# Kernel optimization log

Hardware: AMD Instinct MI355X
Metric: run time of the kernel (lower is better)

Reference implementation:

```python
import jax, jax.numpy as jnp
import numpy as np

VOCAB, EMBED, HIDDEN, NCLS = 50257, 1024, 4096, 3
B, S = 4096, 128


def ternary_quant(w):
    # Per-tensor ternary quantization: scale = mean |w|, weights in {-s, 0, +s}.
    s = jnp.mean(jnp.abs(w))
    return jnp.round(jnp.clip(w / s, -1.0, 1.0)) * s


def layer_norm(x, g, b, eps=1e-5):
    mu = jnp.mean(x, axis=-1, keepdims=True)
    var = jnp.mean(jnp.square(x - mu), axis=-1, keepdims=True)
    return (x - mu) * jax.lax.rsqrt(var + eps) * g + b


def setup_inputs() -> dict:
    key = jax.random.key(0)
    ks = jax.random.split(key, 12)
    input_ids = jax.random.randint(ks[0], (B, S), 0, VOCAB, dtype=jnp.int32)
    emb = jax.random.normal(ks[1], (VOCAB, EMBED), dtype=jnp.float32) * 0.02
    emb = emb.at[0].set(0.0)  # padding_idx=0
    w1 = jax.random.normal(ks[2], (HIDDEN, EMBED), dtype=jnp.float32) * 0.02
    b1 = jnp.zeros((HIDDEN,), jnp.float32)
    w2 = jax.random.normal(ks[3], (HIDDEN // 2, HIDDEN), dtype=jnp.float32) * 0.02
    b2 = jnp.zeros((HIDDEN // 2,), jnp.float32)
    w3 = jax.random.normal(ks[4], (NCLS, HIDDEN // 2), dtype=jnp.float32) * 0.02
    b3 = jnp.zeros((NCLS,), jnp.float32)
    g1 = jnp.ones((HIDDEN,), jnp.float32)
    beta1 = jnp.zeros((HIDDEN,), jnp.float32)
    g2 = jnp.ones((HIDDEN // 2,), jnp.float32)
    beta2 = jnp.zeros((HIDDEN // 2,), jnp.float32)
    return dict(input_ids=input_ids, emb=emb, w1=w1, b1=b1, w2=w2, b2=b2,
                w3=w3, b3=b3, g1=g1, beta1=beta1, g2=g2, beta2=beta2)


def reference(input_ids, emb, w1, b1, w2, b2, w3, b3, g1, beta1, g2, beta2):
    x = emb[input_ids]                                   # (B, S, E)
    mask = (input_ids != 0).astype(x.dtype)[..., None]   # (B, S, 1)
    x = jnp.sum(x * mask, axis=1) / jnp.clip(jnp.sum(mask, axis=1), 1.0)  # (B, E)
    h = jax.nn.gelu(layer_norm(x @ ternary_quant(w1).T + b1, g1, beta1), approximate=False)
    h = jax.nn.gelu(layer_norm(h @ ternary_quant(w2).T + b2, g2, beta2), approximate=False)
    logits = h @ ternary_quant(w3).T + b3                # (B, 3)
    return logits
```

## Files before the change

kernel.cpp:

```cpp
#include <hip/hip_runtime.h>
#include <cstdint>
#include <cstddef>


#define GAS __attribute__((address_space(1)))
#define LAS __attribute__((address_space(3)))

typedef __bf16 bf16x8 __attribute__((ext_vector_type(8)));
typedef float  f32x4  __attribute__((ext_vector_type(4)));
typedef unsigned short u16x8 __attribute__((ext_vector_type(8)));

__device__ __forceinline__ unsigned short f2bf(float f) {
    unsigned int u = __float_as_uint(f);
    u += 0x7FFFu + ((u >> 16) & 1u);
    return (unsigned short)(u >> 16);
}
__device__ __forceinline__ float bf2f(unsigned short h) {
    return __uint_as_float(((unsigned int)h) << 16);
}

static constexpr int BB = 4096;
static constexpr int SS = 128;
static constexpr int EE = 1024;
static constexpr int HH = 4096;
static constexpr int H2D = 2048;
static constexpr int VOCAB = 50257;

static constexpr size_t OFF_S    = 0;
static constexpr size_t OFF_X    = 4096;
static constexpr size_t SZ_X     = (size_t)BB * EE * 2;
static constexpr size_t OFF_EMBH = OFF_X + SZ_X;
static constexpr size_t SZ_EMBH  = (size_t)VOCAB * EE * 2;
static constexpr size_t OFF_Q1   = OFF_EMBH;
static constexpr size_t OFF_Q2   = OFF_Q1 + (size_t)HH * EE * 2;
static constexpr size_t OFF_C    = OFF_Q2 + (size_t)H2D * HH * 2;
static constexpr size_t OFF_H1   = OFF_EMBH + SZ_EMBH;
static constexpr size_t OFF_H2   = OFF_Q1;


__global__ void zero_sums(double* s) {
    if (threadIdx.x < 3) s[threadIdx.x] = 0.0;
}

__global__ __launch_bounds__(256) void prep_kernel(const float* __restrict__ e,
                                                   unsigned short* __restrict__ o,
                                                   const float* __restrict__ w1,
                                                   const float* __restrict__ w2,
                                                   const float* __restrict__ w3,
                                                   double* __restrict__ sums) {
    const int bid = blockIdx.x;
    const int tid = threadIdx.x;
    if (bid < 4096) {
        const int n8 = (VOCAB * EE) / 8;
        for (int i = bid * 256 + tid; i < n8; i += 4096 * 256) {
            const float4 v0 = ((const float4*)e)[2 * i];
            const float4 v1 = ((const float4*)e)[2 * i + 1];
            union { unsigned short u[8]; uint4 q; } r;
            r.u[0] = f2bf(v0.x); r.u[1] = f2bf(v0.y); r.u[2] = f2bf(v0.z); r.u[3] = f2bf(v0.w);
            r.u[4] = f2bf(v1.x); r.u[5] = f2bf(v1.y); r.u[6] = f2bf(v1.z); r.u[7] = f2bf(v1.w);
            ((uint4*)o)[i] = r.q;
        }
        return;
    }
    const float* w; int n; double* out; int b0; int nb;
    if (bid < 5120)      { w = w1; n = HH * EE;  out = sums + 0; b0 = bid - 4096; nb = 1024; }
    else if (bid < 7168) { w = w2; n = H2D * HH; out = sums + 1; b0 = bid - 5120; nb = 2048; }
    else                 { w = w3; n = 3 * H2D;  out = sums + 2; b0 = bid - 7168; nb = 24;   }
    const int lane = tid & 63, wid = tid >> 6;
    double acc = 0.0;
    for (int i = b0 * 256 + tid; i < n; i += nb * 256)
        acc += (double)fabsf(w[i]);
    for (int off = 32; off; off >>= 1) acc += __shfl_down(acc, off);
    __shared__ double r[4];
    if (lane == 0) r[wid] = acc;
    __syncthreads();
    if (tid == 0) atomicAdd(out, r[0] + r[1] + r[2] + r[3]);
}

__global__ __launch_bounds__(256) void quant_all(const float* __restrict__ w1,
                                                 const float* __restrict__ w2,
                                                 const double* __restrict__ sums,
                                                 unsigned short* __restrict__ q1,
                                                 unsigned short* __restrict__ q2) {
    const int bid = blockIdx.x;
    const float* w; int n; unsigned short* q; int b0; int nb; double ssum; double dn;
    if (bid < 4096) { w = w1; n = HH * EE;  q = q1; b0 = bid;        nb = 4096; ssum = sums[0]; dn = (double)(HH) * EE; }
    else            { w = w2; n = H2D * HH; q = q2; b0 = bid - 4096; nb = 8192; ssum = sums[1]; dn = (double)(H2D) * HH; }
    const float inv_s = (float)(dn / ssum);
    for (int i = b0 * 256 + threadIdx.x; i < n; i += nb * 256) {
        float t = w[i] * inv_s;
        t = fminf(1.f, fmaxf(-1.f, t));
        q[i] = f2bf(rintf(t));
    }
}

__global__ __launch_bounds__(256) void pool_kernel(const int* __restrict__ ids,
                                                   const unsigned short* __restrict__ embh,
                                                   unsigned short* __restrict__ X) {
    const int tid = threadIdx.x;
    const int row = tid >> 7;
    const int t   = tid & 127;
    __shared__ int sid[256];
    __shared__ int sorted_ids[2][128];
    __shared__ int cnt[2][64];
    __shared__ int pos[2][64];
    __shared__ int nz[2];
    sid[tid] = ids[(size_t)blockIdx.x * 256 + tid];
    if (tid < 128) ((int*)cnt)[tid] = 0;
    if (tid < 2) nz[tid] = 0;
    __syncthreads();
    const int myid = sid[tid];
    const int ph = myid >> 10;
    atomicAdd(&cnt[row][ph], 1);
    if (myid != 0) atomicAdd(&nz[row], 1);
    __syncthreads();
    if (tid < 2) {
        int s = 0;
        #pragma unroll
        for (int p = 0; p < 64; ++p) { pos[tid][p] = s; s += cnt[tid][p]; }
    }
    __syncthreads();
    const int where = atomicAdd(&pos[row][ph], 1);
    sorted_ids[row][where] = myid;
    __syncthreads();

    const int col = t * 8;
    float a[8] = {};
    #pragma unroll 8
    for (int s = 0; s < 128; ++s) {
        const int id = sorted_ids[row][s];
        const u16x8 v = *(const u16x8*)(embh + (size_t)id * EE + col);
        #pragma unroll
        for (int j = 0; j < 8; ++j) a[j] += bf2f(v[j]);
    }
    const int c = nz[row];
    const float inv = 1.f / (float)(c ? c : 1);
    u16x8 ov;
    #pragma unroll
    for (int j = 0; j < 8; ++j) ov[j] = f2bf(a[j] * inv);
    const int b = blockIdx.x * 2 + row;
    *(u16x8*)(X + (size_t)b * EE + col) = ov;
}

__global__ __launch_bounds__(256) void gemm_bt(const unsigned short* __restrict__ A,
                                               const unsigned short* __restrict__ B,
                                               float* __restrict__ C, int M, int N, int K) {
    __shared__ unsigned short sA[128 * 32];
    __shared__ unsigned short sB[128 * 32];
    const int tid  = threadIdx.x;
    const int wid  = tid >> 6;
    const int lane = tid & 63;
    const int wm = wid >> 1, wn = wid & 1;
    const int quad = lane >> 4;
    const int l16  = lane & 15;
    const int mBase = blockIdx.y * 128;
    const int nBase = blockIdx.x * 128;

    f32x4 acc[4][4] = {};

    const int srow = tid >> 2;
    const int scol = (tid & 3) * 8;
    const size_t aOff0 = (size_t)(mBase + srow) * K + scol;
    const size_t aOff1 = aOff0 + (size_t)64 * K;
    const size_t bOff0 = (size_t)(nBase + srow) * K + scol;
    const size_t bOff1 = bOff0 + (size_t)64 * K;
    unsigned short* ldsA0 = &sA[wid * 512];
    unsigned short* ldsA1 = &sA[2048 + wid * 512];
    unsigned short* ldsB0 = &sB[wid * 512];
    unsigned short* ldsB1 = &sB[2048 + wid * 512];

    for (int k0 = 0; k0 < K; k0 += 32) {
        __syncthreads();
        __builtin_amdgcn_global_load_lds((const GAS void*)(A + aOff0 + k0), (LAS void*)ldsA0, 16, 0, 0);
        __builtin_amdgcn_global_load_lds((const GAS void*)(A + aOff1 + k0), (LAS void*)ldsA1, 16, 0, 0);
        __builtin_amdgcn_global_load_lds((const GAS void*)(B + bOff0 + k0), (LAS void*)ldsB0, 16, 0, 0);
        __builtin_amdgcn_global_load_lds((const GAS void*)(B + bOff1 + k0), (LAS void*)ldsB1, 16, 0, 0);
        __syncthreads();

        bf16x8 af[4], bfr[4];
        #pragma unroll
        for (int i = 0; i < 4; ++i) {
            const int rowA = wm * 64 + i * 16 + l16;
            af[i]  = *(const bf16x8*)(&sA[rowA * 32 + quad * 8]);
            const int rowB = wn * 64 + i * 16 + l16;
            bfr[i] = *(const bf16x8*)(&sB[rowB * 32 + quad * 8]);
        }
        #pragma unroll
        for (int i = 0; i < 4; ++i)
            #pragma unroll
            for (int j = 0; j < 4; ++j)
                acc[i][j] = __builtin_amdgcn_mfma_f32_16x16x32_bf16(af[i], bfr[j], acc[i][j], 0, 0, 0);
    }

    #pragma unroll
    for (int i = 0; i < 4; ++i) {
        const int row0 = mBase + wm * 64 + i * 16 + quad * 4;
        #pragma unroll
        for (int j = 0; j < 4; ++j) {
            const int col = nBase + wn * 64 + j * 16 + l16;
            #pragma unroll
            for (int r = 0; r < 4; ++r)
                C[(size_t)(row0 + r) * N + col] = acc[i][j][r];
        }
    }
}

__global__ __launch_bounds__(256) void ln_gelu_kernel(const float* __restrict__ Cm,
                                                      const double* __restrict__ ssum, double nw,
                                                      const float* __restrict__ bias,
                                                      const float* __restrict__ gamma,
                                                      const float* __restrict__ beta,
                                                      unsigned short* __restrict__ H, int N) {
    __shared__ float buf[4096];
    __shared__ float redS[4], redQ[4];
    const int row = blockIdx.x, tid = threadIdx.x;
    const int lane = tid & 63, wid = tid >> 6;
    const float s = (float)(ssum[0] / nw);
    float ps = 0.f, pq = 0.f;
    for (int c = tid; c < N; c += 256) {
        const float y = Cm[(size_t)row * N + c] * s + bias[c];
        buf[c] = y;
        ps += y; pq += y * y;
    }
    for (int o = 32; o; o >>= 1) { ps += __shfl_down(ps, o); pq += __shfl_down(pq, o); }
    if (lane == 0) { redS[wid] = ps; redQ[wid] = pq; }
    __syncthreads();
    const float sum = redS[0] + redS[1] + redS[2] + redS[3];
    const float sq  = redQ[0] + redQ[1] + redQ[2] + redQ[3];
    const float mu  = sum / (float)N;
    float var = sq / (float)N - mu * mu;
    var = fmaxf(var, 0.f);
    const float inv = rsqrtf(var + 1e-5f);
    for (int c = tid; c < N; c += 256) {
        const float y = (buf[c] - mu) * inv * gamma[c] + beta[c];
        const float g = 0.5f * y * (1.f + erff(y * 0.70710678118654752f));
        H[(size_t)row * N + c] = f2bf(g);
    }
}

__global__ __launch_bounds__(256) void final_kernel(const unsigned short* __restrict__ H2,
                                                    const float* __restrict__ w3,
                                                    const double* __restrict__ ssum,
                                                    const float* __restrict__ b3,
                                                    float* __restrict__ out) {
    const int row = blockIdx.x, tid = threadIdx.x;
    const int lane = tid & 63, wid = tid >> 6;
    const float inv_s3 = (float)((double)(3 * H2D) / ssum[0]);
    float a0 = 0.f, a1 = 0.f, a2 = 0.f;
    for (int k = tid; k < H2D; k += 256) {
        const float h = bf2f(H2[(size_t)row * H2D + k]);
        const float q0 = rintf(fminf(1.f, fmaxf(-1.f, w3[k] * inv_s3)));
        const float q1 = rintf(fminf(1.f, fmaxf(-1.f, w3[H2D + k] * inv_s3)));
        const float q2 = rintf(fminf(1.f, fmaxf(-1.f, w3[2 * H2D + k] * inv_s3)));
        a0 += h * q0; a1 += h * q1; a2 += h * q2;
    }
    for (int o = 32; o; o >>= 1) {
        a0 += __shfl_down(a0, o); a1 += __shfl_down(a1, o); a2 += __shfl_down(a2, o);
    }
    __shared__ float r[3][4];
    if (lane == 0) { r[0][wid] = a0; r[1][wid] = a1; r[2][wid] = a2; }
    __syncthreads();
    if (tid < 3) {
        const float s3 = (float)(ssum[0] / (double)(3 * H2D));
        out[(size_t)row * 3 + tid] =
            (r[tid][0] + r[tid][1] + r[tid][2] + r[tid][3]) * s3 + b3[tid];
    }
}


extern "C" void kernel_launch(void* const* d_in, const int* in_sizes, int n_in,
                              void* d_out, int out_size, void* d_ws, size_t ws_size,
                              hipStream_t stream) {
    const int*   ids = (const int*)d_in[0];
    const float* emb = (const float*)d_in[1];
    const float* w1  = (const float*)d_in[2];
    const float* b1  = (const float*)d_in[3];
    const float* w2  = (const float*)d_in[4];
    const float* b2  = (const float*)d_in[5];
    const float* w3  = (const float*)d_in[6];
    const float* b3  = (const float*)d_in[7];
    const float* g1  = (const float*)d_in[8];
    const float* be1 = (const float*)d_in[9];
    const float* g2  = (const float*)d_in[10];
    const float* be2 = (const float*)d_in[11];
    float* out = (float*)d_out;
    char* ws = (char*)d_ws;

    double*         sums = (double*)(ws + OFF_S);
    unsigned short* X    = (unsigned short*)(ws + OFF_X);
    unsigned short* embh = (unsigned short*)(ws + OFF_EMBH);
    unsigned short* q1   = (unsigned short*)(ws + OFF_Q1);
    unsigned short* q2   = (unsigned short*)(ws + OFF_Q2);
    float*          Cbuf = (float*)(ws + OFF_C);
    unsigned short* H1   = (unsigned short*)(ws + OFF_H1);
    unsigned short* H2   = (unsigned short*)(ws + OFF_H2);

    zero_sums<<<1, 64, 0, stream>>>(sums);
    prep_kernel<<<7192, 256, 0, stream>>>(emb, embh, w1, w2, w3, sums);
    pool_kernel<<<BB / 2, 256, 0, stream>>>(ids, embh, X);

    quant_all<<<12288, 256, 0, stream>>>(w1, w2, sums, q1, q2);

    gemm_bt<<<dim3(HH / 128, BB / 128), 256, 0, stream>>>(X, q1, Cbuf, BB, HH, EE);
    ln_gelu_kernel<<<BB, 256, 0, stream>>>(Cbuf, sums + 0, (double)HH * (double)EE,
                                           b1, g1, be1, H1, HH);
    gemm_bt<<<dim3(H2D / 128, BB / 128), 256, 0, stream>>>(H1, q2, Cbuf, BB, H2D, HH);
    ln_gelu_kernel<<<BB, 256, 0, stream>>>(Cbuf, sums + 1, (double)H2D * (double)HH,
                                           b2, g2, be2, H2, H2D);
    final_kernel<<<BB, 256, 0, stream>>>(H2, w3, sums + 2, b3, out);
}
```

Before: 723.0 us.

## Gather fp32 embeddings directly and drop full-vocab bf16 conversion pass

Removes the pass that converted the whole 50257x1024 embedding table to bf16 and instead has the pooling kernel read fp32 rows directly, sorting ids with finer buckets for locality. The weight abs-sum reduction becomes a two-stage deterministic partial-sum reduction with float4 loads instead of double atomics, and quantization processes eight elements per thread with vectorized loads and stores. This avoids reading and writing roughly 300MB for the table conversion, at the cost of doubling the bytes gathered per embedding row during pooling.

```diff
diff --git a/kernel.cpp b/kernel.cpp
--- a/kernel.cpp
+++ b/kernel.cpp
@@ -27,54 +27,54 @@
 static constexpr int VOCAB = 50257;
 
 static constexpr size_t OFF_S    = 0;
-static constexpr size_t OFF_X    = 4096;
-static constexpr size_t SZ_X     = (size_t)BB * EE * 2;
-static constexpr size_t OFF_EMBH = OFF_X + SZ_X;
-static constexpr size_t SZ_EMBH  = (size_t)VOCAB * EE * 2;
-static constexpr size_t OFF_Q1   = OFF_EMBH;
+static constexpr size_t OFF_X    = 16384;
+static constexpr size_t OFF_Q1   = OFF_X + (size_t)BB * EE * 2;
 static constexpr size_t OFF_Q2   = OFF_Q1 + (size_t)HH * EE * 2;
 static constexpr size_t OFF_C    = OFF_Q2 + (size_t)H2D * HH * 2;
-static constexpr size_t OFF_H1   = OFF_EMBH + SZ_EMBH;
-static constexpr size_t OFF_H2   = OFF_Q1;
-
-
-__global__ void zero_sums(double* s) {
-    if (threadIdx.x < 3) s[threadIdx.x] = 0.0;
-}
-
-__global__ __launch_bounds__(256) void prep_kernel(const float* __restrict__ e,
-                                                   unsigned short* __restrict__ o,
-                                                   const float* __restrict__ w1,
-                                                   const float* __restrict__ w2,
+static constexpr size_t OFF_H1   = OFF_C + (size_t)BB * HH * 4;
+static constexpr size_t OFF_H2   = OFF_X;
+
+
+__global__ __launch_bounds__(256) void absum_part(const float* __restrict__ w1,
+                                                  const float* __restrict__ w2,
+                                                  double* __restrict__ part) {
+    const int bid = blockIdx.x;
+    const float* w; int n4; int b0; int nb;
+    if (bid < 512) { w = w1; n4 = HH * EE / 4;  b0 = bid;       nb = 512;  }
+    else           { w = w2; n4 = H2D * HH / 4; b0 = bid - 512; nb = 1024; }
+    const int tid = threadIdx.x;
+    const int lane = tid & 63, wid = tid >> 6;
+    double acc = 0.0;
+    for (int i = b0 * 256 + tid; i < n4; i += nb * 256) {
+        const float4 v = ((const float4*)w)[i];
+        acc += (double)fabsf(v.x) + (double)fabsf(v.y) +
+               (double)fabsf(v.z) + (double)fabsf(v.w);
+    }
+    for (int o = 32; o; o >>= 1) acc += __shfl_down(acc, o);
+    __shared__ double r[4];
+    if (lane == 0) r[wid] = acc;
+    __syncthreads();
+    if (tid == 0) part[bid] = r[0] + r[1] + r[2] + r[3];
+}
+
+__global__ __launch_bounds__(256) void reduce_sums(const double* __restrict__ part,
                                                    const float* __restrict__ w3,
                                                    double* __restrict__ sums) {
-    const int bid = blockIdx.x;
-    const int tid = threadIdx.x;
-    if (bid < 4096) {
-        const int n8 = (VOCAB * EE) / 8;
-        for (int i = bid * 256 + tid; i < n8; i += 4096 * 256) {
-            const float4 v0 = ((const float4*)e)[2 * i];
-            const float4 v1 = ((const float4*)e)[2 * i + 1];
-            union { unsigned short u[8]; uint4 q; } r;
-            r.u[0] = f2bf(v0.x); r.u[1] = f2bf(v0.y); r.u[2] = f2bf(v0.z); r.u[3] = f2bf(v0.w);
-            r.u[4] = f2bf(v1.x); r.u[5] = f2bf(v1.y); r.u[6] = f2bf(v1.z); r.u[7] = f2bf(v1.w);
-            ((uint4*)o)[i] = r.q;
-        }
-        return;
-    }
-    const float* w; int n; double* out; int b0; int nb;
-    if (bid < 5120)      { w = w1; n = HH * EE;  out = sums + 0; b0 = bid - 4096; nb = 1024; }
-    else if (bid < 7168) { w = w2; n = H2D * HH; out = sums + 1; b0 = bid - 5120; nb = 2048; }
-    else                 { w = w3; n = 3 * H2D;  out = sums + 2; b0 = bid - 7168; nb = 24;   }
+    const int bid = blockIdx.x, tid = threadIdx.x;
     const int lane = tid & 63, wid = tid >> 6;
     double acc = 0.0;
-    for (int i = b0 * 256 + tid; i < n; i += nb * 256)
-        acc += (double)fabsf(w[i]);
-    for (int off = 32; off; off >>= 1) acc += __shfl_down(acc, off);
+    if (bid == 0) {
+        acc = part[tid] + part[tid + 256];
+    } else if (bid == 1) {
+        acc = part[512 + tid] + part[768 + tid] + part[1024 + tid] + part[1280 + tid];
+    } else {
+        for (int i = tid; i < 3 * H2D; i += 256) acc += (double)fabsf(w3[i]);
+    }
+    for (int o = 32; o; o >>= 1) acc += __shfl_down(acc, o);
     __shared__ double r[4];
     if (lane == 0) r[wid] = acc;
     __syncthreads();
-    if (tid == 0) atomicAdd(out, r[0] + r[1] + r[2] + r[3]);
+    if (tid == 0) sums[bid] = r[0] + r[1] + r[2] + r[3];
 }
 
 __global__ __launch_bounds__(256) void quant_all(const float* __restrict__ w1,
@@ -83,41 +83,46 @@
                                                  unsigned short* __restrict__ q1,
                                                  unsigned short* __restrict__ q2) {
     const int bid = blockIdx.x;
-    const float* w; int n; unsigned short* q; int b0; int nb; double ssum; double dn;
-    if (bid < 4096) { w = w1; n = HH * EE;  q = q1; b0 = bid;        nb = 4096; ssum = sums[0]; dn = (double)(HH) * EE; }
-    else            { w = w2; n = H2D * HH; q = q2; b0 = bid - 4096; nb = 8192; ssum = sums[1]; dn = (double)(H2D) * HH; }
+    const float* w; int n8; unsigned short* q; int b0; int nb; double ssum; double dn;
+    if (bid < 2048) { w = w1; n8 = HH * EE / 8;  q = q1; b0 = bid;        nb = 2048; ssum = sums[0]; dn = (double)HH * EE;  }
+    else            { w = w2; n8 = H2D * HH / 8; q = q2; b0 = bid - 2048; nb = 4096; ssum = sums[1]; dn = (double)H2D * HH; }
     const float inv_s = (float)(dn / ssum);
-    for (int i = b0 * 256 + threadIdx.x; i < n; i += nb * 256) {
-        float t = w[i] * inv_s;
-        t = fminf(1.f, fmaxf(-1.f, t));
-        q[i] = f2bf(rintf(t));
+    for (int i = b0 * 256 + threadIdx.x; i < n8; i += nb * 256) {
+        const float4 v0 = ((const float4*)w)[2 * i];
+        const float4 v1 = ((const float4*)w)[2 * i + 1];
+        union { unsigned short u[8]; uint4 p; } r;
+        const float a[8] = {v0.x, v0.y, v0.z, v0.w, v1.x, v1.y, v1.z, v1.w};
+        #pragma unroll
+        for (int j = 0; j < 8; ++j)
+            r.u[j] = f2bf(rintf(fminf(1.f, fmaxf(-1.f, a[j] * inv_s))));
+        ((uint4*)q)[i] = r.p;
     }
 }
 
 __global__ __launch_bounds__(256) void pool_kernel(const int* __restrict__ ids,
-                                                   const unsigned short* __restrict__ embh,
+                                                   const float* __restrict__ emb,
                                                    unsigned short* __restrict__ X) {
     const int tid = threadIdx.x;
     const int row = tid >> 7;
     const int t   = tid & 127;
     __shared__ int sid[256];
     __shared__ int sorted_ids[2][128];
-    __shared__ int cnt[2][64];
-    __shared__ int pos[2][64];
+    __shared__ int cnt[2][128];
+    __shared__ int pos[2][128];
     __shared__ int nz[2];
     sid[tid] = ids[(size_t)blockIdx.x * 256 + tid];
-    if (tid < 128) ((int*)cnt)[tid] = 0;
+    cnt[row][t] = 0;
     if (tid < 2) nz[tid] = 0;
     __syncthreads();
     const int myid = sid[tid];
-    const int ph = myid >> 10;
+    const int ph = myid >> 9;
     atomicAdd(&cnt[row][ph], 1);
     if (myid != 0) atomicAdd(&nz[row], 1);
     __syncthreads();
     if (tid < 2) {
         int s = 0;
         #pragma unroll
-        for (int p = 0; p < 64; ++p) { pos[tid][p] = s; s += cnt[tid][p]; }
+        for (int p = 0; p < 128; ++p) { pos[tid][p] = s; s += cnt[tid][p]; }
     }
     __syncthreads();
     const int where = atomicAdd(&pos[row][ph], 1);
@@ -129,9 +134,11 @@
     #pragma unroll 8
     for (int s = 0; s < 128; ++s) {
         const int id = sorted_ids[row][s];
-        const u16x8 v = *(const u16x8*)(embh + (size_t)id * EE + col);
-        #pragma unroll
-        for (int j = 0; j < 8; ++j) a[j] += bf2f(v[j]);
+        const float4* p = (const float4*)(emb + (size_t)id * EE + col);
+        const float4 v0 = p[0];
+        const float4 v1 = p[1];
+        a[0] += v0.x; a[1] += v0.y; a[2] += v0.z; a[3] += v0.w;
+        a[4] += v1.x; a[5] += v1.y; a[6] += v1.z; a[7] += v1.w;
     }
     const int c = nz[row];
     const float inv = 1.f / (float)(c ? c : 1);
@@ -287,19 +294,20 @@
     char* ws = (char*)d_ws;
 
     double*         sums = (double*)(ws + OFF_S);
+    double*         part = sums + 8;
     unsigned short* X    = (unsigned short*)(ws + OFF_X);
-    unsigned short* embh = (unsigned short*)(ws + OFF_EMBH);
     unsigned short* q1   = (unsigned short*)(ws + OFF_Q1);
     unsigned short* q2   = (unsigned short*)(ws + OFF_Q2);
     float*          Cbuf = (float*)(ws + OFF_C);
     unsigned short* H1   = (unsigned short*)(ws + OFF_H1);
     unsigned short* H2   = (unsigned short*)(ws + OFF_H2);
 
-    zero_sums<<<1, 64, 0, stream>>>(sums);
-    prep_kernel<<<7192, 256, 0, stream>>>(emb, embh, w1, w2, w3, sums);
-    pool_kernel<<<BB / 2, 256, 0, stream>>>(ids, embh, X);
-
-    quant_all<<<12288, 256, 0, stream>>>(w1, w2, sums, q1, q2);
+    absum_part<<<1536, 256, 0, stream>>>(w1, w2, part);
+    reduce_sums<<<3, 256, 0, stream>>>(part, w3, sums);
+
+    pool_kernel<<<BB / 2, 256, 0, stream>>>(ids, emb, X);
+
+    quant_all<<<6144, 256, 0, stream>>>(w1, w2, sums, q1, q2);
 
     gemm_bt<<<dim3(HH / 128, BB / 128), 256, 0, stream>>>(X, q1, Cbuf, BB, HH, EE);
     ln_gelu_kernel<<<BB, 256, 0, stream>>>(Cbuf, sums + 0, (double)HH * (double)EE,
```

Result: slower. 808.5 us (+11.8%).
